# Kernel tuning notes

Hardware: AMD Instinct MI355X
Metric: run time of the kernel (lower is better)

The kernel has to match this reference:

```python
import jax, jax.numpy as jnp
import numpy as np

H = 1024   # hidden_dim
C = 256    # numchars
T = 512    # total_timesteps
LAM = 0.05


def setup_inputs() -> dict:
    key = jax.random.key(0)
    ks = jax.random.split(key, 32)
    s = np.float32(1.0 / np.sqrt(H))
    n = lambda k, shape, sc=s: jax.random.normal(k, shape, dtype=jnp.float32) * sc
    inp = {
        'x': jax.random.uniform(ks[0], (T, C), dtype=jnp.float32),
        # layer 1 state unit (LSTM in=2H) + V: H->C (softmaxed)
        'W_ih_1': n(ks[1], (4 * H, 2 * H)), 'W_hh_1': n(ks[2], (4 * H, H)),
        'b_ih_1': n(ks[3], (4 * H,)), 'b_hh_1': n(ks[4], (4 * H,)),
        'Vw_1': n(ks[5], (C, H)), 'Vb_1': n(ks[6], (C,)),
        # layer 2 state unit (LSTM in=2H) + V: H->H
        'W_ih_2': n(ks[7], (4 * H, 2 * H)), 'W_hh_2': n(ks[8], (4 * H, H)),
        'b_ih_2': n(ks[9], (4 * H,)), 'b_hh_2': n(ks[10], (4 * H,)),
        'Vw_2': n(ks[11], (H, H)), 'Vb_2': n(ks[12], (H,)),
        # layer 3 (top) state unit (LSTM in=H) + V: H->H
        'W_ih_3': n(ks[13], (4 * H, H)), 'W_hh_3': n(ks[14], (4 * H, H)),
        'b_ih_3': n(ks[15], (4 * H,)), 'b_hh_3': n(ks[16], (4 * H,)),
        'Vw_3': n(ks[17], (H, H)), 'Vb_3': n(ks[18], (H,)),
        # error-unit W projections (layers 0..2; top layer's err unit is never run)
        'Ww_0': n(ks[19], (H, C)), 'Wb_0': n(ks[20], (H,)),
        'Ww_1': n(ks[21], (H, H)), 'Wb_1': n(ks[22], (H,)),
        'Ww_2': n(ks[23], (H, H)), 'Wb_2': n(ks[24], (H,)),
        # initial recon vectors (torch init: randn; layer 1 gets softmax in forward)
        'r1': n(ks[25], (C,), 1.0), 'r2': n(ks[26], (H,), 1.0), 'r3': n(ks[27], (H,), 1.0),
        'iternumber': 0,
    }
    return inp


def _lstm_cell(x, h, c, Wih, Whh, bih, bhh):
    g = Wih @ x + bih + Whh @ h + bhh  # [4H], torch gate order i,f,g,o
    i, f, gg, o = jnp.split(g, 4)
    c2 = jax.nn.sigmoid(f) * c + jax.nn.sigmoid(i) * jnp.tanh(gg)
    return jax.nn.sigmoid(o) * jnp.tanh(c2), c2


def reference(x, W_ih_1, W_hh_1, b_ih_1, b_hh_1, Vw_1, Vb_1,
              W_ih_2, W_hh_2, b_ih_2, b_hh_2, Vw_2, Vb_2,
              W_ih_3, W_hh_3, b_ih_3, b_hh_3, Vw_3, Vb_3,
              Ww_0, Wb_0, Ww_1, Wb_1, Ww_2, Wb_2, r1, r2, r3, iternumber):
    zH = jnp.zeros((H,), jnp.float32)

    def step(carry, x_t):
        h1, c1, h2, c2, h3, c3, rec1, rec2, rec3, TD1, TD2, loss, fll = carry
        # lyr 0: state := input char; err unit 0 uses layer-1 recon (previous t)
        s0 = x_t
        u = s0 * jnp.log(rec1) + (1.0 - s0) * jnp.log(1.0 - rec1)
        TD0 = s0 - rec1
        loss0 = -jnp.sum(u)
        BU0 = Ww_0 @ TD0 + Wb_0
        # lyr 1: state unit consumes fresh BU0 and stale TD1, then err unit 1
        h1n, c1n = _lstm_cell(jnp.concatenate([BU0, TD1]), h1, c1, W_ih_1, W_hh_1, b_ih_1, b_hh_1)
        rec1n = jax.nn.softmax(Vw_1 @ h1n + Vb_1)
        TD1n = h1n - rec2
        BU1 = Ww_1 @ TD1n + Wb_1
        # lyr 2
        h2n, c2n = _lstm_cell(jnp.concatenate([BU1, TD2]), h2, c2, W_ih_2, W_hh_2, b_ih_2, b_hh_2)
        rec2n = Vw_2 @ h2n + Vb_2
        TD2n = h2n - rec3
        BU2 = Ww_2 @ TD2n + Wb_2
        # lyr 3 (top): LSTM input is BU2 only; its err unit never runs (TD3 == 0)
        h3n, c3n = _lstm_cell(BU2, h3, c3, W_ih_3, W_hh_3, b_ih_3, b_hh_3)
        rec3n = Vw_3 @ h3n + Vb_3
        loss = loss + loss0 + LAM * jnp.sum(jnp.abs(TD1n)) + (LAM * LAM) * jnp.sum(jnp.abs(TD2n))
        fll = fll + loss0
        new = (h1n, c1n, h2n, c2n, h3n, c3n, rec1n, rec2n, rec3n, TD1n, TD2n, loss, fll)
        return new, rec1n  # prediction at t is layer-1 recon

    init = (zH, zH, zH, zH, zH, zH,
            jax.nn.softmax(r1), r2, r3,  # init recons (layer 1 softmaxed, per init_vars)
            zH, zH, jnp.float32(0.0), jnp.float32(0.0))
    carry, predictions = jax.lax.scan(step, init, x)
    loss, first_layer_loss = carry[-2], carry[-1]
    return loss, first_layer_loss, predictions
```

## Files before the change

### kernel.cpp

```cpp
#include <hip/hip_runtime.h>
#include <math.h>

#define HD 1024
#define CD 256
#define TT 512
#define GD 4096
#define NWG 256
#define NTH 1024
#define WPB 16
#define NWAVE (NWG*WPB)
#define LAMF 0.05f
#define SMEMB (4 * WPB * HD * 2)

typedef unsigned long long ull;
typedef unsigned short ushortt;
typedef _Float16 hh2 __attribute__((ext_vector_type(2)));

__device__ __align__(16) ushortt hM1[GD * CD];
__device__ __align__(16) ushortt hM2[GD * HD];
__device__ __align__(16) ushortt hM3[GD * HD];
__device__ __align__(16) ushortt hW1b[GD * HD];
__device__ __align__(16) ushortt hWhh1[GD * HD];
__device__ __align__(16) ushortt hW2b[GD * HD];
__device__ __align__(16) ushortt hWhh2[GD * HD];
__device__ __align__(16) ushortt hWhh3[GD * HD];
__device__ __align__(16) ushortt hVw1[CD * HD];
__device__ __align__(16) ushortt hVw2[HD * HD];
__device__ __align__(16) ushortt hVw3[HD * HD];

__device__ __align__(16) float d_g1[GD], d_g2[GD], d_g3[GD];
__device__ __align__(16) float d_z1[CD];
__device__ __align__(16) float d_rec2[HD], d_rec3[HD];
__device__ int d_arr[NWG][32];
__device__ int d_rel;

__global__ void pc_init() { d_arr[threadIdx.x][0] = 0; if (threadIdx.x == 0) d_rel = 0; }

__device__ __forceinline__ float sigf(float x)     { return 1.f / (1.f + __expf(-x)); }
__device__ __forceinline__ float tanhfast(float x) { return 1.f - 2.f / (1.f + __expf(2.f * x)); }

__device__ __forceinline__ ushortt f2h(float x) {
  union { ushortt u; _Float16 h; } c; c.h = (_Float16)x; return c.u;
}
__device__ __forceinline__ float h2f(ushortt u) {
  union { ushortt u; _Float16 h; } c; c.u = u; return (float)c.h;
}
__device__ __forceinline__ unsigned packh2(float a, float b) {
  union { unsigned u; hh2 h; } c; c.h = hh2{(_Float16)a, (_Float16)b}; return c.u;
}
__device__ __forceinline__ float fd2(unsigned a, unsigned b, float c) {
  union { unsigned u; hh2 h; } ua, ub; ua.u = a; ub.u = b;
  return __builtin_amdgcn_fdot2(ua.h, ub.h, c, false);
}

__device__ __forceinline__ float cload(const float* p) {
  return __hip_atomic_load(p, __ATOMIC_RELAXED, __HIP_MEMORY_SCOPE_AGENT);
}
__device__ __forceinline__ void cstore(float* p, float v) {
  __hip_atomic_store(p, v, __ATOMIC_RELAXED, __HIP_MEMORY_SCOPE_AGENT);
}
__device__ __forceinline__ float2 cload2(const float* p) {
  union { ull u; float2 f; } c;
  c.u = __hip_atomic_load((const ull*)p, __ATOMIC_RELAXED, __HIP_MEMORY_SCOPE_AGENT);
  return c.f;
}

__device__ __forceinline__ void gbar(int& ep) {
  ++ep;
  __syncthreads();
  const int tid = threadIdx.x;
  if (blockIdx.x == 0) {
    if (tid >= 1 && tid < NWG) {
      while (__hip_atomic_load(&d_arr[tid][0], __ATOMIC_RELAXED, __HIP_MEMORY_SCOPE_AGENT) < ep)
        __builtin_amdgcn_s_sleep(1);
    }
    __syncthreads();
    if (tid == 0)
      __hip_atomic_store(&d_rel, ep, __ATOMIC_RELEASE, __HIP_MEMORY_SCOPE_AGENT);
  } else {
    if (tid == 0) {
      __hip_atomic_store(&d_arr[blockIdx.x][0], ep, __ATOMIC_RELEASE, __HIP_MEMORY_SCOPE_AGENT);
      while (__hip_atomic_load(&d_rel, __ATOMIC_RELAXED, __HIP_MEMORY_SCOPE_AGENT) < ep)
        __builtin_amdgcn_s_sleep(1);
    }
    __syncthreads();
  }
}

__device__ __forceinline__ float wredsum(float v) {
  #pragma unroll
  for (int off = 32; off; off >>= 1) v += __shfl_xor(v, off);
  return v;
}
__device__ __forceinline__ float wredmax(float v) {
  #pragma unroll
  for (int off = 32; off; off >>= 1) v = fmaxf(v, __shfl_xor(v, off));
  return v;
}

__device__ __forceinline__ float dotp(const float* __restrict__ w, const float* xv, int n, int lane) {
  float a0 = 0.f, a1 = 0.f, a2 = 0.f, a3 = 0.f;
  for (int c = lane * 4; c < n; c += 256) {
    const float4 wv = *(const float4*)(w + c);
    const float4 vv = *(const float4*)(xv + c);
    a0 = fmaf(wv.x, vv.x, a0); a1 = fmaf(wv.y, vv.y, a1);
    a2 = fmaf(wv.z, vv.z, a2); a3 = fmaf(wv.w, vv.w, a3);
  }
  return (a0 + a1) + (a2 + a3);
}

__device__ __forceinline__ float dotH(const ushortt* __restrict__ w, const ushortt* xv, int lane) {
  const uint4 w0 = *(const uint4*)(w + lane * 8);
  const uint4 w1 = *(const uint4*)(w + lane * 8 + 512);
  const uint4 v0 = *(const uint4*)(xv + lane * 8);
  const uint4 v1 = *(const uint4*)(xv + lane * 8 + 512);
  float a = 0.f;
  a = fd2(w0.x, v0.x, a); a = fd2(w0.y, v0.y, a);
  a = fd2(w0.z, v0.z, a); a = fd2(w0.w, v0.w, a);
  a = fd2(w1.x, v1.x, a); a = fd2(w1.y, v1.y, a);
  a = fd2(w1.z, v1.z, a); a = fd2(w1.w, v1.w, a);
  return a;
}
__device__ __forceinline__ float dotH256(const ushortt* __restrict__ w, const ushortt* xv, int lane) {
  const uint2 wv = *(const uint2*)(w + lane * 4);
  const uint2 vv = *(const uint2*)(xv + lane * 4);
  float a = fd2(wv.x, vv.x, 0.f);
  return fd2(wv.y, vv.y, a);
}

__global__ __launch_bounds__(256) void pc_conv(
    const float* __restrict__ Wih1, const float* __restrict__ Whh1,
    const float* __restrict__ Wih2, const float* __restrict__ Whh2,
    const float* __restrict__ Whh3, const float* __restrict__ Vw1,
    const float* __restrict__ Vw2,  const float* __restrict__ Vw3) {
  const size_t stride = (size_t)gridDim.x * 256;
  const size_t i0 = (size_t)blockIdx.x * 256 + threadIdx.x;
  for (size_t i = i0; i < (size_t)GD * HD; i += stride) {
    size_t r = i >> 10, c = i & 1023;
    size_t src = (r << 11) + HD + c;
    hW1b[i]  = f2h(Wih1[src]);
    hW2b[i]  = f2h(Wih2[src]);
    hWhh1[i] = f2h(Whh1[i]);
    hWhh2[i] = f2h(Whh2[i]);
    hWhh3[i] = f2h(Whh3[i]);
  }
  for (size_t i = i0; i < (size_t)HD * HD; i += stride) {
    hVw2[i] = f2h(Vw2[i]);
    hVw3[i] = f2h(Vw3[i]);
  }
  for (size_t i = i0; i < (size_t)CD * HD; i += stride) hVw1[i] = f2h(Vw1[i]);
}

__global__ __launch_bounds__(256) void pc_fold(
    const float* __restrict__ Wih1, const float* __restrict__ Wih2,
    const float* __restrict__ Wih3, const float* __restrict__ Ww0,
    const float* __restrict__ Ww1,  const float* __restrict__ Ww2) {
  int b = blockIdx.x;
  const float* A; const float* B; ushortt* C; int N, lda;
  if (b < 256)        { A = Wih1; B = Ww0; C = hM1; N = CD; lda = 2 * HD; }
  else if (b < 1280)  { A = Wih2; B = Ww1; C = hM2; N = HD; lda = 2 * HD; b -= 256; }
  else                { A = Wih3; B = Ww2; C = hM3; N = HD; lda = HD;     b -= 1280; }
  const int ctiles = N >> 6;
  const int rt = b / ctiles, ct = b - rt * ctiles;
  const int tid = threadIdx.x;
  const int tx = tid & 15, ty = tid >> 4;

  __shared__ float sA[16][65];
  __shared__ float sB[16][64];

  float acc[4][4] = {};
  const int ar = tid >> 2, aq = tid & 3;
  const int br = tid >> 4, bq = tid & 15;

  for (int kk = 0; kk < HD; kk += 16) {
    float4 av = *(const float4*)(A + (size_t)(rt * 64 + ar) * lda + kk + aq * 4);
    float4 bv = *(const float4*)(B + (size_t)(kk + br) * N + ct * 64 + bq * 4);
    __syncthreads();
    sA[aq * 4 + 0][ar] = av.x; sA[aq * 4 + 1][ar] = av.y;
    sA[aq * 4 + 2][ar] = av.z; sA[aq * 4 + 3][ar] = av.w;
    *(float4*)&sB[br][bq * 4] = bv;
    __syncthreads();
    #pragma unroll
    for (int k = 0; k < 16; ++k) {
      const float4 b4 = *(const float4*)&sB[k][tx * 4];
      const float a0 = sA[k][ty * 4 + 0], a1 = sA[k][ty * 4 + 1];
      const float a2 = sA[k][ty * 4 + 2], a3 = sA[k][ty * 4 + 3];
      acc[0][0] = fmaf(a0, b4.x, acc[0][0]); acc[0][1] = fmaf(a0, b4.y, acc[0][1]);
      acc[0][2] = fmaf(a0, b4.z, acc[0][2]); acc[0][3] = fmaf(a0, b4.w, acc[0][3]);
      acc[1][0] = fmaf(a1, b4.x, acc[1][0]); acc[1][1] = fmaf(a1, b4.y, acc[1][1]);
      acc[1][2] = fmaf(a1, b4.z, acc[1][2]); acc[1][3] = fmaf(a1, b4.w, acc[1][3]);
      acc[2][0] = fmaf(a2, b4.x, acc[2][0]); acc[2][1] = fmaf(a2, b4.y, acc[2][1]);
      acc[2][2] = fmaf(a2, b4.z, acc[2][2]); acc[2][3] = fmaf(a2, b4.w, acc[2][3]);
      acc[3][0] = fmaf(a3, b4.x, acc[3][0]); acc[3][1] = fmaf(a3, b4.y, acc[3][1]);
      acc[3][2] = fmaf(a3, b4.z, acc[3][2]); acc[3][3] = fmaf(a3, b4.w, acc[3][3]);
    }
  }
  #pragma unroll
  for (int i = 0; i < 4; ++i) {
    uint2 r = make_uint2(packh2(acc[i][0], acc[i][1]), packh2(acc[i][2], acc[i][3]));
    *(uint2*)(C + (size_t)(rt * 64 + ty * 4 + i) * N + ct * 64 + tx * 4) = r;
  }
}

__global__ __launch_bounds__(NTH, 1) void pc_main(
    const float* __restrict__ x,
    const float* __restrict__ Wih1, const float* __restrict__ Whh1,
    const float* __restrict__ bih1, const float* __restrict__ bhh1,
    const float* __restrict__ Vw1,  const float* __restrict__ Vb1,
    const float* __restrict__ Wih2, const float* __restrict__ Whh2,
    const float* __restrict__ bih2, const float* __restrict__ bhh2,
    const float* __restrict__ Vw2,  const float* __restrict__ Vb2,
    const float* __restrict__ Wih3, const float* __restrict__ Whh3,
    const float* __restrict__ bih3, const float* __restrict__ bhh3,
    const float* __restrict__ Vw3,  const float* __restrict__ Vb3,
    const float* __restrict__ Ww0,  const float* __restrict__ Wb0,
    const float* __restrict__ Ww1,  const float* __restrict__ Wb1,
    const float* __restrict__ Ww2,  const float* __restrict__ Wb2,
    const float* __restrict__ r1,   const float* __restrict__ r2,
    const float* __restrict__ r3,
    float* __restrict__ out) {
  const int tid  = threadIdx.x;
  const int lane = tid & 63;
  const int bid  = blockIdx.x;
  const int wv   = tid >> 6;
  const int wid  = bid * WPB + wv;
  const bool iswg0 = (bid == 0);
  const bool w0    = iswg0 && tid < 64;

  extern __shared__ __align__(16) ushortt smem[];
  ushortt* sM2 = smem;
  ushortt* sW2 = sM2 + WPB * HD;
  ushortt* sH2 = sW2 + WPB * HD;
  ushortt* sM3 = sH2 + WPB * HD;

  __shared__ __align__(16) ushortt s_h1[HD], s_TD1[HD], s_h2[HD], s_TD2[HD], s_h3[HD];
  __shared__ __align__(16) float s_c1[HD], s_c2[HD], s_c3[HD];
  __shared__ __align__(16) ushortt s_small[CD];

  const int e = (tid < 512) ? (((tid + (bid << 3)) & 511) * 2) : 0;

  const int jR = ((wid & 3) == 1)  ? (wid >> 2) : -1;
  const int jZ = ((wid & 15) == 2) ? (wid >> 4) : -1;

  int ep = 0;
  float loss_acc = 0.f, fll_acc = 0.f;
  float b1, b2, b3, vbR3 = 0.f, vbR2 = 0.f, vbZ = 0.f;

  {
    const uint4* gM2 = (const uint4*)(hM2   + (size_t)wid * HD);
    const uint4* gW2 = (const uint4*)(hW2b  + (size_t)wid * HD);
    const uint4* gH2 = (const uint4*)(hWhh2 + (size_t)wid * HD);
    const uint4* gM3 = (const uint4*)(hM3   + (size_t)wid * HD);
    uint4* lM2 = (uint4*)(sM2 + wv * HD);
    uint4* lW2 = (uint4*)(sW2 + wv * HD);
    uint4* lH2 = (uint4*)(sH2 + wv * HD);
    uint4* lM3 = (uint4*)(sM3 + wv * HD);
    #pragma unroll
    for (int i = 0; i < 2; ++i) {
      lM2[lane + 64 * i] = gM2[lane + 64 * i];
      lW2[lane + 64 * i] = gW2[lane + 64 * i];
      lH2[lane + 64 * i] = gH2[lane + 64 * i];
      lM3[lane + 64 * i] = gM3[lane + 64 * i];
    }
  }
  if (tid < 512) {
    int j = tid * 2;
    *(float2*)(s_c1 + j) = *(const float2*)(Wb0 + j);
    *(float2*)(s_c2 + j) = *(const float2*)(Wb1 + j);
    *(float2*)(s_c3 + j) = *(const float2*)(Wb2 + j);
  }
  __syncthreads();
  b1 = bih1[wid] + bhh1[wid] + wredsum(dotp(Wih1 + (size_t)wid * 2 * HD, s_c1, HD, lane));
  b2 = bih2[wid] + bhh2[wid] + wredsum(dotp(Wih2 + (size_t)wid * 2 * HD, s_c2, HD, lane));
  b3 = bih3[wid] + bhh3[wid] + wredsum(dotp(Wih3 + (size_t)wid * HD,     s_c3, HD, lane));
  if (jR >= 0) { vbR3 = Vb3[jR]; vbR2 = Vb2[jR]; }
  if (jZ >= 0) vbZ = Vb1[jZ];
  __syncthreads();
  if (tid < 512) {
    int j = tid * 2;
    const float2 z2 = make_float2(0.f, 0.f);
    *(float2*)(s_c1 + j) = z2; *(float2*)(s_c2 + j) = z2; *(float2*)(s_c3 + j) = z2;
    *(unsigned*)(s_h1 + j) = 0u; *(unsigned*)(s_TD1 + j) = 0u;
    *(unsigned*)(s_h2 + j) = 0u; *(unsigned*)(s_TD2 + j) = 0u;
    *(unsigned*)(s_h3 + j) = 0u;
  }
  if (tid < 64) {
    float4 z4 = *(const float4*)(r1 + tid * 4);
    float m = wredmax(fmaxf(fmaxf(z4.x, z4.y), fmaxf(z4.z, z4.w)));
    float e0 = __expf(z4.x - m), e1 = __expf(z4.y - m);
    float e2 = __expf(z4.z - m), e3 = __expf(z4.w - m);
    float inv = 1.f / wredsum((e0 + e1) + (e2 + e3));
    float p0 = e0 * inv, p1 = e1 * inv, p2 = e2 * inv, p3 = e3 * inv;
    float4 xv = *(const float4*)(x + tid * 4);
    *(uint2*)(s_small + tid * 4) =
        make_uint2(packh2(xv.x - p0, xv.y - p1), packh2(xv.z - p2, xv.w - p3));
    if (iswg0) {
      float u = xv.x * __logf(p0) + (1.f - xv.x) * __logf(1.f - p0)
              + xv.y * __logf(p1) + (1.f - xv.y) * __logf(1.f - p1)
              + xv.z * __logf(p2) + (1.f - xv.z) * __logf(1.f - p2)
              + xv.w * __logf(p3) + (1.f - xv.w) * __logf(1.f - p3);
      u = wredsum(u);
      if (tid == 0) { loss_acc -= u; fll_acc -= u; }
    }
  }
  __syncthreads();
  {
    float s = wredsum(dotH256(hM1 + (size_t)wid * CD, s_small, lane));
    if (lane == 0) cstore(&d_g1[wid], s + b1);
  }
  gbar(ep);

  for (int t = 0; t < TT; ++t) {
    if (tid < 512) {
      if (t > 0) {
        float2 gi = cload2(&d_g3[e]),          gf = cload2(&d_g3[e + HD]);
        float2 gg = cload2(&d_g3[e + 2 * HD]), go = cload2(&d_g3[e + 3 * HD]);
        float cA = sigf(gf.x) * s_c3[e]     + sigf(gi.x) * tanhfast(gg.x);
        float cB = sigf(gf.y) * s_c3[e + 1] + sigf(gi.y) * tanhfast(gg.y);
        float hA = sigf(go.x) * tanhfast(cA);
        float hB = sigf(go.y) * tanhfast(cB);
        s_c3[e] = cA; s_c3[e + 1] = cB;
        *(unsigned*)(s_h3 + e) = packh2(hA, hB);
      }
      {
        float2 gi = cload2(&d_g1[e]),          gf = cload2(&d_g1[e + HD]);
        float2 gg = cload2(&d_g1[e + 2 * HD]), go = cload2(&d_g1[e + 3 * HD]);
        float2 rc = (t == 0) ? *(const float2*)(r2 + e) : cload2(&d_rec2[e]);
        float cA = sigf(gf.x) * s_c1[e]     + sigf(gi.x) * tanhfast(gg.x);
        float cB = sigf(gf.y) * s_c1[e + 1] + sigf(gi.y) * tanhfast(gg.y);
        float hA = sigf(go.x) * tanhfast(cA);
        float hB = sigf(go.y) * tanhfast(cB);
        s_c1[e] = cA; s_c1[e + 1] = cB;
        *(unsigned*)(s_h1 + e)  = packh2(hA, hB);
        *(unsigned*)(s_TD1 + e) = packh2(hA - rc.x, hB - rc.y);
      }
    }
    __syncthreads();
    if (w0) {
      float a = 0.f;
      #pragma unroll
      for (int k = 0; k < 16; ++k) a += fabsf(h2f(s_TD1[tid + 64 * k]));
      a = wredsum(a);
      if (tid == 0) loss_acc += LAMF * a;
    }
    {
      float s = dotH(sM2 + wv * HD, s_TD1, lane)
              + dotH(sW2 + wv * HD, s_TD2, lane)
              + dotH(sH2 + wv * HD, s_h2,  lane);
      s = wredsum(s);
      if (lane == 0) cstore(&d_g2[wid], s + b2);
    }
    if (t > 0 && jR >= 0) {
      float s = wredsum(dotH(hVw3 + (size_t)jR * HD, s_h3, lane));
      if (lane == 0) cstore(&d_rec3[jR], s + vbR3);
    }
    if (jZ >= 0) {
      float s = wredsum(dotH(hVw1 + (size_t)jZ * HD, s_h1, lane));
      if (lane == 0) cstore(&d_z1[jZ], s + vbZ);
    }
    gbar(ep);

    if (tid < 512) {
      float2 gi = cload2(&d_g2[e]),          gf = cload2(&d_g2[e + HD]);
      float2 gg = cload2(&d_g2[e + 2 * HD]), go = cload2(&d_g2[e + 3 * HD]);
      float2 rc = (t == 0) ? *(const float2*)(r3 + e) : cload2(&d_rec3[e]);
      float cA = sigf(gf.x) * s_c2[e]     + sigf(gi.x) * tanhfast(gg.x);
      float cB = sigf(gf.y) * s_c2[e + 1] + sigf(gi.y) * tanhfast(gg.y);
      float hA = sigf(go.x) * tanhfast(cA);
      float hB = sigf(go.y) * tanhfast(cB);
      s_c2[e] = cA; s_c2[e + 1] = cB;
      *(unsigned*)(s_h2 + e)  = packh2(hA, hB);
      *(unsigned*)(s_TD2 + e) = packh2(hA - rc.x, hB - rc.y);
    }
    if (tid < 64) {
      float2 za = cload2(&d_z1[tid * 4]), zb = cload2(&d_z1[tid * 4 + 2]);
      float m = wredmax(fmaxf(fmaxf(za.x, za.y), fmaxf(zb.x, zb.y)));
      float e0 = __expf(za.x - m), e1 = __expf(za.y - m);
      float e2 = __expf(zb.x - m), e3 = __expf(zb.y - m);
      float inv = 1.f / wredsum((e0 + e1) + (e2 + e3));
      float p0 = e0 * inv, p1 = e1 * inv, p2 = e2 * inv, p3 = e3 * inv;
      if (t < TT - 1) {
        float4 xv = *(const float4*)(x + (size_t)(t + 1) * CD + tid * 4);
        *(uint2*)(s_small + tid * 4) =
            make_uint2(packh2(xv.x - p0, xv.y - p1), packh2(xv.z - p2, xv.w - p3));
        if (iswg0) {
          float u = xv.x * __logf(p0) + (1.f - xv.x) * __logf(1.f - p0)
                  + xv.y * __logf(p1) + (1.f - xv.y) * __logf(1.f - p1)
                  + xv.z * __logf(p2) + (1.f - xv.z) * __logf(1.f - p2)
                  + xv.w * __logf(p3) + (1.f - xv.w) * __logf(1.f - p3);
          u = wredsum(u);
          if (tid == 0) { loss_acc -= u; fll_acc -= u; }
        }
      }
      if (iswg0) {
        float* po = out + 2 + (size_t)t * CD + tid * 4;
        po[0] = p0; po[1] = p1; po[2] = p2; po[3] = p3;
      }
    }
    __syncthreads();
    if (w0) {
      float a = 0.f;
      #pragma unroll
      for (int k = 0; k < 16; ++k) a += fabsf(h2f(s_TD2[tid + 64 * k]));
      a = wredsum(a);
      if (tid == 0) loss_acc += (LAMF * LAMF) * a;
    }
    if (t < TT - 1) {
      {
        float s = dotH(sM3 + wv * HD, s_TD2, lane)
                + dotH(hWhh3 + (size_t)wid * HD, s_h3, lane);
        s = wredsum(s);
        if (lane == 0) cstore(&d_g3[wid], s + b3);
      }
      {
        float s = dotH256(hM1 + (size_t)wid * CD, s_small, lane)
                + dotH(hW1b  + (size_t)wid * HD, s_TD1, lane)
                + dotH(hWhh1 + (size_t)wid * HD, s_h1,  lane);
        s = wredsum(s);
        if (lane == 0) cstore(&d_g1[wid], s + b1);
      }
      if (jR >= 0) {
        float s = wredsum(dotH(hVw2 + (size_t)jR * HD, s_h2, lane));
        if (lane == 0) cstore(&d_rec2[jR], s + vbR2);
      }
      gbar(ep);
    }
  }

  if (iswg0 && tid == 0) { out[0] = loss_acc; out[1] = fll_acc; }
}

extern "C" void kernel_launch(void* const* d_in, const int* in_sizes, int n_in,
                              void* d_out, int out_size, void* d_ws, size_t ws_size,
                              hipStream_t stream) {
  const float* x    = (const float*)d_in[0];
  const float* Wih1 = (const float*)d_in[1];
  const float* Whh1 = (const float*)d_in[2];
  const float* bih1 = (const float*)d_in[3];
  const float* bhh1 = (const float*)d_in[4];
  const float* Vw1  = (const float*)d_in[5];
  const float* Vb1  = (const float*)d_in[6];
  const float* Wih2 = (const float*)d_in[7];
  const float* Whh2 = (const float*)d_in[8];
  const float* bih2 = (const float*)d_in[9];
  const float* bhh2 = (const float*)d_in[10];
  const float* Vw2  = (const float*)d_in[11];
  const float* Vb2  = (const float*)d_in[12];
  const float* Wih3 = (const float*)d_in[13];
  const float* Whh3 = (const float*)d_in[14];
  const float* bih3 = (const float*)d_in[15];
  const float* bhh3 = (const float*)d_in[16];
  const float* Vw3  = (const float*)d_in[17];
  const float* Vb3  = (const float*)d_in[18];
  const float* Ww0  = (const float*)d_in[19];
  const float* Wb0  = (const float*)d_in[20];
  const float* Ww1  = (const float*)d_in[21];
  const float* Wb1  = (const float*)d_in[22];
  const float* Ww2  = (const float*)d_in[23];
  const float* Wb2  = (const float*)d_in[24];
  const float* r1   = (const float*)d_in[25];
  const float* r2   = (const float*)d_in[26];
  const float* r3   = (const float*)d_in[27];

  static int smem_set = 0;
  if (!smem_set) {
    hipFuncSetAttribute((const void*)pc_main,
                        hipFuncAttributeMaxDynamicSharedMemorySize, SMEMB);
    smem_set = 1;
  }

  pc_conv<<<1024, 256, 0, stream>>>(Wih1, Whh1, Wih2, Whh2, Whh3, Vw1, Vw2, Vw3);
  pc_fold<<<2304, 256, 0, stream>>>(Wih1, Wih2, Wih3, Ww0, Ww1, Ww2);
  pc_init<<<1, NWG, 0, stream>>>();
  pc_main<<<NWG, NTH, SMEMB, stream>>>(x, Wih1, Whh1, bih1, bhh1, Vw1, Vb1,
                                       Wih2, Whh2, bih2, bhh2, Vw2, Vb2,
                                       Wih3, Whh3, bih3, bhh3, Vw3, Vb3,
                                       Ww0, Wb0, Ww1, Wb1, Ww2, Wb2,
                                       r1, r2, r3, (float*)d_out);
}
```

Before: 8.420 ms.

## Make each workgroup own four hidden units' gates and exchange fp16 states globally

Rows are remapped so that each workgroup computes all four gates (i,f,g,o) for four hidden units. The LSTM nonlinearities and cell updates therefore run locally from shared memory, and only the packed fp16 h/TD vectors are written to global memory instead of full fp32 gate vectors. Every block then reloads the complete h/TD vectors into shared memory after each barrier, and double-buffers the layer-2 state to avoid read/write races. This shrinks global traffic per step and removes the redundant per-block gate nonlinearity work, at the cost of a serialized single-wave epilogue and extra __syncthreads inside each phase.

```diff
diff --git a/kernel.cpp b/kernel.cpp
--- a/kernel.cpp
+++ b/kernel.cpp
@@ -8,7 +8,6 @@
 #define NWG 256
 #define NTH 1024
 #define WPB 16
-#define NWAVE (NWG*WPB)
 #define LAMF 0.05f
 #define SMEMB (4 * WPB * HD * 2)
 
@@ -28,9 +27,9 @@
 __device__ __align__(16) ushortt hVw2[HD * HD];
 __device__ __align__(16) ushortt hVw3[HD * HD];
 
-__device__ __align__(16) float d_g1[GD], d_g2[GD], d_g3[GD];
+__device__ __align__(8) ushortt d_h1h[HD], d_TD1h[HD], d_h3h[HD];
+__device__ __align__(8) ushortt d_h2h[2][HD], d_TD2h[2][HD];
 __device__ __align__(16) float d_z1[CD];
-__device__ __align__(16) float d_rec2[HD], d_rec3[HD];
 __device__ int d_arr[NWG][32];
 __device__ int d_rel;
 
@@ -63,6 +62,15 @@
   union { ull u; float2 f; } c;
   c.u = __hip_atomic_load((const ull*)p, __ATOMIC_RELAXED, __HIP_MEMORY_SCOPE_AGENT);
   return c.f;
+}
+__device__ __forceinline__ uint2 cloadU2(const ushortt* p) {
+  union { ull u; uint2 v; } c;
+  c.u = __hip_atomic_load((const ull*)p, __ATOMIC_RELAXED, __HIP_MEMORY_SCOPE_AGENT);
+  return c.v;
+}
+__device__ __forceinline__ void cstoreU2(ushortt* p, uint2 v) {
+  union { ull u; uint2 v; } c; c.v = v;
+  __hip_atomic_store((ull*)p, c.u, __ATOMIC_RELAXED, __HIP_MEMORY_SCOPE_AGENT);
 }
 
 __device__ __forceinline__ void gbar(int& ep) {
@@ -223,7 +231,10 @@
   const int lane = tid & 63;
   const int bid  = blockIdx.x;
   const int wv   = tid >> 6;
-  const int wid  = bid * WPB + wv;
+  const int gi   = wv & 3;
+  const int slot = wv >> 2;
+  const int rg   = gi * HD + bid * 4 + slot;
+  const int jown = bid * 4 + slot;
   const bool iswg0 = (bid == 0);
   const bool w0    = iswg0 && tid < 64;
 
@@ -233,24 +244,21 @@
   ushortt* sH2 = sW2 + WPB * HD;
   ushortt* sM3 = sH2 + WPB * HD;
 
-  __shared__ __align__(16) ushortt s_h1[HD], s_TD1[HD], s_h2[HD], s_TD2[HD], s_h3[HD];
-  __shared__ __align__(16) float s_c1[HD], s_c2[HD], s_c3[HD];
+  __shared__ __align__(16) ushortt s_TD1[HD], s_h1[HD], s_TD2[HD], s_h2[HD], s_h3[HD];
   __shared__ __align__(16) ushortt s_small[CD];
-
-  const int e = (tid < 512) ? (((tid + (bid << 3)) & 511) * 2) : 0;
-
-  const int jR = ((wid & 3) == 1)  ? (wid >> 2) : -1;
-  const int jZ = ((wid & 15) == 2) ? (wid >> 4) : -1;
+  __shared__ float s_gateA[WPB], s_gateB[WPB], s_rec[4];
+  __shared__ float s_c1own[4], s_c2own[4], s_c3own[4];
+  __shared__ __align__(16) float s_ftmp[HD];
 
   int ep = 0;
   float loss_acc = 0.f, fll_acc = 0.f;
   float b1, b2, b3, vbR3 = 0.f, vbR2 = 0.f, vbZ = 0.f;
 
   {
-    const uint4* gM2 = (const uint4*)(hM2   + (size_t)wid * HD);
-    const uint4* gW2 = (const uint4*)(hW2b  + (size_t)wid * HD);
-    const uint4* gH2 = (const uint4*)(hWhh2 + (size_t)wid * HD);
-    const uint4* gM3 = (const uint4*)(hM3   + (size_t)wid * HD);
+    const uint4* gM2 = (const uint4*)(hM2   + (size_t)rg * HD);
+    const uint4* gW2 = (const uint4*)(hW2b  + (size_t)rg * HD);
+    const uint4* gH2 = (const uint4*)(hWhh2 + (size_t)rg * HD);
+    const uint4* gM3 = (const uint4*)(hM3   + (size_t)rg * HD);
     uint4* lM2 = (uint4*)(sM2 + wv * HD);
     uint4* lW2 = (uint4*)(sW2 + wv * HD);
     uint4* lH2 = (uint4*)(sH2 + wv * HD);
@@ -263,26 +271,26 @@
       lM3[lane + 64 * i] = gM3[lane + 64 * i];
     }
   }
-  if (tid < 512) {
-    int j = tid * 2;
-    *(float2*)(s_c1 + j) = *(const float2*)(Wb0 + j);
-    *(float2*)(s_c2 + j) = *(const float2*)(Wb1 + j);
-    *(float2*)(s_c3 + j) = *(const float2*)(Wb2 + j);
-  }
-  __syncthreads();
-  b1 = bih1[wid] + bhh1[wid] + wredsum(dotp(Wih1 + (size_t)wid * 2 * HD, s_c1, HD, lane));
-  b2 = bih2[wid] + bhh2[wid] + wredsum(dotp(Wih2 + (size_t)wid * 2 * HD, s_c2, HD, lane));
-  b3 = bih3[wid] + bhh3[wid] + wredsum(dotp(Wih3 + (size_t)wid * HD,     s_c3, HD, lane));
-  if (jR >= 0) { vbR3 = Vb3[jR]; vbR2 = Vb2[jR]; }
-  if (jZ >= 0) vbZ = Vb1[jZ];
-  __syncthreads();
-  if (tid < 512) {
-    int j = tid * 2;
-    const float2 z2 = make_float2(0.f, 0.f);
-    *(float2*)(s_c1 + j) = z2; *(float2*)(s_c2 + j) = z2; *(float2*)(s_c3 + j) = z2;
-    *(unsigned*)(s_h1 + j) = 0u; *(unsigned*)(s_TD1 + j) = 0u;
-    *(unsigned*)(s_h2 + j) = 0u; *(unsigned*)(s_TD2 + j) = 0u;
-    *(unsigned*)(s_h3 + j) = 0u;
+  if (tid < 512) *(float2*)(s_ftmp + tid * 2) = *(const float2*)(Wb0 + tid * 2);
+  __syncthreads();
+  b1 = bih1[rg] + bhh1[rg] + wredsum(dotp(Wih1 + (size_t)rg * 2 * HD, s_ftmp, HD, lane));
+  __syncthreads();
+  if (tid < 512) *(float2*)(s_ftmp + tid * 2) = *(const float2*)(Wb1 + tid * 2);
+  __syncthreads();
+  b2 = bih2[rg] + bhh2[rg] + wredsum(dotp(Wih2 + (size_t)rg * 2 * HD, s_ftmp, HD, lane));
+  __syncthreads();
+  if (tid < 512) *(float2*)(s_ftmp + tid * 2) = *(const float2*)(Wb2 + tid * 2);
+  __syncthreads();
+  b3 = bih3[rg] + bhh3[rg] + wredsum(dotp(Wih3 + (size_t)rg * HD, s_ftmp, HD, lane));
+  if (gi == 0) vbR3 = Vb3[jown];
+  if (gi == 2) vbR2 = Vb2[jown];
+  if (wv == 1) vbZ  = Vb1[bid];
+  if (tid < 4) { s_c2own[tid] = 0.f; s_c3own[tid] = 0.f; }
+  if (tid == 0) {
+    uint2 z2 = make_uint2(0u, 0u);
+    cstoreU2(d_h2h[1] + bid * 4, z2);
+    cstoreU2(d_TD2h[1] + bid * 4, z2);
+    cstoreU2(d_h3h + bid * 4, z2);
   }
   if (tid < 64) {
     float4 z4 = *(const float4*)(r1 + tid * 4);
@@ -305,125 +313,174 @@
   }
   __syncthreads();
   {
-    float s = wredsum(dotH256(hM1 + (size_t)wid * CD, s_small, lane));
-    if (lane == 0) cstore(&d_g1[wid], s + b1);
+    float s = wredsum(dotH256(hM1 + (size_t)rg * CD, s_small, lane)) + b1;
+    if (lane == 0) s_gateA[wv] = s;
+  }
+  __syncthreads();
+  if (tid < 64) {
+    float h = 0.f, td = 0.f;
+    if (lane < 4) {
+      float gI = s_gateA[lane * 4 + 0], gF = s_gateA[lane * 4 + 1];
+      float gG = s_gateA[lane * 4 + 2], gO = s_gateA[lane * 4 + 3];
+      (void)gF;
+      float cn = sigf(gI) * tanhfast(gG);
+      h  = sigf(gO) * tanhfast(cn);
+      td = h - r2[bid * 4 + lane];
+      s_c1own[lane] = cn;
+    }
+    uint2 uh, ut;
+    uh.x = packh2(__shfl(h, 0), __shfl(h, 1));  uh.y = packh2(__shfl(h, 2), __shfl(h, 3));
+    ut.x = packh2(__shfl(td, 0), __shfl(td, 1)); ut.y = packh2(__shfl(td, 2), __shfl(td, 3));
+    if (lane == 0) { cstoreU2(d_h1h + bid * 4, uh); cstoreU2(d_TD1h + bid * 4, ut); }
   }
   gbar(ep);
 
   for (int t = 0; t < TT; ++t) {
-    if (tid < 512) {
-      if (t > 0) {
-        float2 gi = cload2(&d_g3[e]),          gf = cload2(&d_g3[e + HD]);
-        float2 gg = cload2(&d_g3[e + 2 * HD]), go = cload2(&d_g3[e + 3 * HD]);
-        float cA = sigf(gf.x) * s_c3[e]     + sigf(gi.x) * tanhfast(gg.x);
-        float cB = sigf(gf.y) * s_c3[e + 1] + sigf(gi.y) * tanhfast(gg.y);
-        float hA = sigf(go.x) * tanhfast(cA);
-        float hB = sigf(go.y) * tanhfast(cB);
-        s_c3[e] = cA; s_c3[e + 1] = cB;
-        *(unsigned*)(s_h3 + e) = packh2(hA, hB);
+    const int pb = t & 1, pbm = pb ^ 1;
+
+    {
+      const int grp = tid >> 8, k = tid & 255;
+      if (grp == 0) {
+        *(uint2*)(s_TD1 + k * 4) = cloadU2(d_TD1h + k * 4);
+        *(uint2*)(s_h1 + k * 4)  = cloadU2(d_h1h + k * 4);
+      } else if (grp == 1) {
+        *(uint2*)(s_TD2 + k * 4) = cloadU2(d_TD2h[pbm] + k * 4);
+      } else if (grp == 2) {
+        *(uint2*)(s_h2 + k * 4)  = cloadU2(d_h2h[pbm] + k * 4);
+      } else {
+        *(uint2*)(s_h3 + k * 4)  = cloadU2(d_h3h + k * 4);
+      }
+      __syncthreads();
+      if (w0) {
+        float a = 0.f;
+        #pragma unroll
+        for (int kk = 0; kk < 16; ++kk) a += fabsf(h2f(s_TD1[tid + 64 * kk]));
+        a = wredsum(a);
+        if (tid == 0) loss_acc += LAMF * a;
       }
       {
-        float2 gi = cload2(&d_g1[e]),          gf = cload2(&d_g1[e + HD]);
-        float2 gg = cload2(&d_g1[e + 2 * HD]), go = cload2(&d_g1[e + 3 * HD]);
-        float2 rc = (t == 0) ? *(const float2*)(r2 + e) : cload2(&d_rec2[e]);
-        float cA = sigf(gf.x) * s_c1[e]     + sigf(gi.x) * tanhfast(gg.x);
-        float cB = sigf(gf.y) * s_c1[e + 1] + sigf(gi.y) * tanhfast(gg.y);
-        float hA = sigf(go.x) * tanhfast(cA);
-        float hB = sigf(go.y) * tanhfast(cB);
-        s_c1[e] = cA; s_c1[e + 1] = cB;
-        *(unsigned*)(s_h1 + e)  = packh2(hA, hB);
-        *(unsigned*)(s_TD1 + e) = packh2(hA - rc.x, hB - rc.y);
-      }
-    }
-    __syncthreads();
-    if (w0) {
-      float a = 0.f;
-      #pragma unroll
-      for (int k = 0; k < 16; ++k) a += fabsf(h2f(s_TD1[tid + 64 * k]));
-      a = wredsum(a);
-      if (tid == 0) loss_acc += LAMF * a;
-    }
+        float s = dotH(sM2 + wv * HD, s_TD1, lane)
+                + dotH(sW2 + wv * HD, s_TD2, lane)
+                + dotH(sH2 + wv * HD, s_h2,  lane);
+        s = wredsum(s);
+        if (lane == 0) s_gateA[wv] = s + b2;
+      }
+      if (gi == 0) {
+        if (t > 0) {
+          float s = wredsum(dotH(hVw3 + (size_t)jown * HD, s_h3, lane)) + vbR3;
+          if (lane == 0) s_rec[slot] = s;
+        } else if (lane == 0) s_rec[slot] = r3[jown];
+      }
+      if (wv == 1) {
+        float s = wredsum(dotH(hVw1 + (size_t)bid * HD, s_h1, lane)) + vbZ;
+        if (lane == 0) cstore(&d_z1[bid], s);
+      }
+      __syncthreads();
+      if (tid < 64) {
+        float h = 0.f, td = 0.f;
+        if (lane < 4) {
+          float gI = s_gateA[lane * 4 + 0], gF = s_gateA[lane * 4 + 1];
+          float gG = s_gateA[lane * 4 + 2], gO = s_gateA[lane * 4 + 3];
+          float cn = sigf(gF) * s_c2own[lane] + sigf(gI) * tanhfast(gG);
+          h  = sigf(gO) * tanhfast(cn);
+          td = h - s_rec[lane];
+          s_c2own[lane] = cn;
+        }
+        uint2 uh, ut;
+        uh.x = packh2(__shfl(h, 0), __shfl(h, 1));  uh.y = packh2(__shfl(h, 2), __shfl(h, 3));
+        ut.x = packh2(__shfl(td, 0), __shfl(td, 1)); ut.y = packh2(__shfl(td, 2), __shfl(td, 3));
+        if (lane == 0) { cstoreU2(d_h2h[pb] + bid * 4, uh); cstoreU2(d_TD2h[pb] + bid * 4, ut); }
+      }
+    }
+    gbar(ep);
+
     {
-      float s = dotH(sM2 + wv * HD, s_TD1, lane)
-              + dotH(sW2 + wv * HD, s_TD2, lane)
-              + dotH(sH2 + wv * HD, s_h2,  lane);
-      s = wredsum(s);
-      if (lane == 0) cstore(&d_g2[wid], s + b2);
-    }
-    if (t > 0 && jR >= 0) {
-      float s = wredsum(dotH(hVw3 + (size_t)jR * HD, s_h3, lane));
-      if (lane == 0) cstore(&d_rec3[jR], s + vbR3);
-    }
-    if (jZ >= 0) {
-      float s = wredsum(dotH(hVw1 + (size_t)jZ * HD, s_h1, lane));
-      if (lane == 0) cstore(&d_z1[jZ], s + vbZ);
-    }
-    gbar(ep);
-
-    if (tid < 512) {
-      float2 gi = cload2(&d_g2[e]),          gf = cload2(&d_g2[e + HD]);
-      float2 gg = cload2(&d_g2[e + 2 * HD]), go = cload2(&d_g2[e + 3 * HD]);
-      float2 rc = (t == 0) ? *(const float2*)(r3 + e) : cload2(&d_rec3[e]);
-      float cA = sigf(gf.x) * s_c2[e]     + sigf(gi.x) * tanhfast(gg.x);
-      float cB = sigf(gf.y) * s_c2[e + 1] + sigf(gi.y) * tanhfast(gg.y);
-      float hA = sigf(go.x) * tanhfast(cA);
-      float hB = sigf(go.y) * tanhfast(cB);
-      s_c2[e] = cA; s_c2[e + 1] = cB;
-      *(unsigned*)(s_h2 + e)  = packh2(hA, hB);
-      *(unsigned*)(s_TD2 + e) = packh2(hA - rc.x, hB - rc.y);
-    }
-    if (tid < 64) {
-      float2 za = cload2(&d_z1[tid * 4]), zb = cload2(&d_z1[tid * 4 + 2]);
-      float m = wredmax(fmaxf(fmaxf(za.x, za.y), fmaxf(zb.x, zb.y)));
-      float e0 = __expf(za.x - m), e1 = __expf(za.y - m);
-      float e2 = __expf(zb.x - m), e3 = __expf(zb.y - m);
-      float inv = 1.f / wredsum((e0 + e1) + (e2 + e3));
-      float p0 = e0 * inv, p1 = e1 * inv, p2 = e2 * inv, p3 = e3 * inv;
+      const int grp = tid >> 8, k = tid & 255;
+      if (grp == 0)      *(uint2*)(s_TD2 + k * 4) = cloadU2(d_TD2h[pb] + k * 4);
+      else if (grp == 1) *(uint2*)(s_h2 + k * 4)  = cloadU2(d_h2h[pb] + k * 4);
+      if (tid < 64) {
+        float2 za = cload2(&d_z1[tid * 4]), zb = cload2(&d_z1[tid * 4 + 2]);
+        float m = wredmax(fmaxf(fmaxf(za.x, za.y), fmaxf(zb.x, zb.y)));
+        float e0 = __expf(za.x - m), e1 = __expf(za.y - m);
+        float e2 = __expf(zb.x - m), e3 = __expf(zb.y - m);
+        float inv = 1.f / wredsum((e0 + e1) + (e2 + e3));
+        float p0 = e0 * inv, p1 = e1 * inv, p2 = e2 * inv, p3 = e3 * inv;
+        if (t < TT - 1) {
+          float4 xv = *(const float4*)(x + (size_t)(t + 1) * CD + tid * 4);
+          *(uint2*)(s_small + tid * 4) =
+              make_uint2(packh2(xv.x - p0, xv.y - p1), packh2(xv.z - p2, xv.w - p3));
+          if (iswg0) {
+            float u = xv.x * __logf(p0) + (1.f - xv.x) * __logf(1.f - p0)
+                    + xv.y * __logf(p1) + (1.f - xv.y) * __logf(1.f - p1)
+                    + xv.z * __logf(p2) + (1.f - xv.z) * __logf(1.f - p2)
+                    + xv.w * __logf(p3) + (1.f - xv.w) * __logf(1.f - p3);
+            u = wredsum(u);
+            if (tid == 0) { loss_acc -= u; fll_acc -= u; }
+          }
+        }
+        if (iswg0) {
+          float* po = out + 2 + (size_t)t * CD + tid * 4;
+          po[0] = p0; po[1] = p1; po[2] = p2; po[3] = p3;
+        }
+      }
+      __syncthreads();
+      if (w0) {
+        float a = 0.f;
+        #pragma unroll
+        for (int kk = 0; kk < 16; ++kk) a += fabsf(h2f(s_TD2[tid + 64 * kk]));
+        a = wredsum(a);
+        if (tid == 0) loss_acc += (LAMF * LAMF) * a;
+      }
       if (t < TT - 1) {
-        float4 xv = *(const float4*)(x + (size_t)(t + 1) * CD + tid * 4);
-        *(uint2*)(s_small + tid * 4) =
-            make_uint2(packh2(xv.x - p0, xv.y - p1), packh2(xv.z - p2, xv.w - p3));
-        if (iswg0) {
-          float u = xv.x * __logf(p0) + (1.f - xv.x) * __logf(1.f - p0)
-                  + xv.y * __logf(p1) + (1.f - xv.y) * __logf(1.f - p1)
-                  + xv.z * __logf(p2) + (1.f - xv.z) * __logf(1.f - p2)
-                  + xv.w * __logf(p3) + (1.f - xv.w) * __logf(1.f - p3);
-          u = wredsum(u);
-          if (tid == 0) { loss_acc -= u; fll_acc -= u; }
-        }
-      }
-      if (iswg0) {
-        float* po = out + 2 + (size_t)t * CD + tid * 4;
-        po[0] = p0; po[1] = p1; po[2] = p2; po[3] = p3;
-      }
-    }
-    __syncthreads();
-    if (w0) {
-      float a = 0.f;
-      #pragma unroll
-      for (int k = 0; k < 16; ++k) a += fabsf(h2f(s_TD2[tid + 64 * k]));
-      a = wredsum(a);
-      if (tid == 0) loss_acc += (LAMF * LAMF) * a;
-    }
-    if (t < TT - 1) {
-      {
-        float s = dotH(sM3 + wv * HD, s_TD2, lane)
-                + dotH(hWhh3 + (size_t)wid * HD, s_h3, lane);
-        s = wredsum(s);
-        if (lane == 0) cstore(&d_g3[wid], s + b3);
-      }
-      {
-        float s = dotH256(hM1 + (size_t)wid * CD, s_small, lane)
-                + dotH(hW1b  + (size_t)wid * HD, s_TD1, lane)
-                + dotH(hWhh1 + (size_t)wid * HD, s_h1,  lane);
-        s = wredsum(s);
-        if (lane == 0) cstore(&d_g1[wid], s + b1);
-      }
-      if (jR >= 0) {
-        float s = wredsum(dotH(hVw2 + (size_t)jR * HD, s_h2, lane));
-        if (lane == 0) cstore(&d_rec2[jR], s + vbR2);
-      }
-      gbar(ep);
+        {
+          float s = dotH(sM3 + wv * HD, s_TD2, lane)
+                  + dotH(hWhh3 + (size_t)rg * HD, s_h3, lane);
+          s = wredsum(s);
+          if (lane == 0) s_gateB[wv] = s + b3;
+        }
+        {
+          float s = dotH256(hM1 + (size_t)rg * CD, s_small, lane)
+                  + dotH(hW1b  + (size_t)rg * HD, s_TD1, lane)
+                  + dotH(hWhh1 + (size_t)rg * HD, s_h1,  lane);
+          s = wredsum(s);
+          if (lane == 0) s_gateA[wv] = s + b1;
+        }
+        if (gi == 2) {
+          float s = wredsum(dotH(hVw2 + (size_t)jown * HD, s_h2, lane)) + vbR2;
+          if (lane == 0) s_rec[slot] = s;
+        }
+        __syncthreads();
+        if (tid < 64) {
+          float h3n = 0.f, h1n = 0.f, td1 = 0.f;
+          if (lane < 4) {
+            {
+              float gI = s_gateB[lane * 4 + 0], gF = s_gateB[lane * 4 + 1];
+              float gG = s_gateB[lane * 4 + 2], gO = s_gateB[lane * 4 + 3];
+              float cn = sigf(gF) * s_c3own[lane] + sigf(gI) * tanhfast(gG);
+              h3n = sigf(gO) * tanhfast(cn);
+              s_c3own[lane] = cn;
+            }
+            {
+              float gI = s_gateA[lane * 4 + 0], gF = s_gateA[lane * 4 + 1];
+              float gG = s_gateA[lane * 4 + 2], gO = s_gateA[lane * 4 + 3];
+              float cn = sigf(gF) * s_c1own[lane] + sigf(gI) * tanhfast(gG);
+              h1n = sigf(gO) * tanhfast(cn);
+              td1 = h1n - s_rec[lane];
+              s_c1own[lane] = cn;
+            }
+          }
+          uint2 u3, u1, utd;
+          u3.x = packh2(__shfl(h3n, 0), __shfl(h3n, 1)); u3.y = packh2(__shfl(h3n, 2), __shfl(h3n, 3));
+          u1.x = packh2(__shfl(h1n, 0), __shfl(h1n, 1)); u1.y = packh2(__shfl(h1n, 2), __shfl(h1n, 3));
+          utd.x = packh2(__shfl(td1, 0), __shfl(td1, 1)); utd.y = packh2(__shfl(td1, 2), __shfl(td1, 3));
+          if (lane == 0) {
+            cstoreU2(d_h3h + bid * 4, u3);
+            cstoreU2(d_h1h + bid * 4, u1);
+            cstoreU2(d_TD1h + bid * 4, utd);
+          }
+        }
+        gbar(ep);
+      }
     }
   }
 
```

New measurement: 7.692 ms. 8.6% less time.
